# Kernel tuning notes

Hardware: AMD Instinct MI355X
Metric: run time of the kernel (lower is better)

## Reference

```python
import jax, jax.numpy as jnp
import numpy as np

H = 0.1  # spatial delta h from init kwargs


def _stencils():
    k_avg = jnp.array([[0., 0., 0.], [0., 1., 0.], [0., 0., 0.]], jnp.float32)
    k_x = (0.5 / H) * jnp.array([[0., -1., 0.], [0., 0., 0.], [0., 1., 0.]], jnp.float32)
    k_y = (0.5 / H) * jnp.array([[0., 0., 0.], [-1., 0., 1.], [0., 0., 0.]], jnp.float32)
    k_xx = (1.0 / H ** 2) * jnp.array([[0., 1., 0.], [0., -2., 0.], [0., 1., 0.]], jnp.float32)
    k_yy = (1.0 / H ** 2) * jnp.array([[0., 0., 0.], [1., -2., 1.], [0., 0., 0.]], jnp.float32)
    return k_avg, k_x, k_y, k_xx, k_yy


def setup_inputs() -> dict:
    key = jax.random.key(0)
    ks = jax.random.split(key, 11)
    B = 65536
    inp = {
        'data': jax.random.normal(ks[0], (B, 3, 11, 11), jnp.float32),
        'mix_a': jax.random.normal(ks[1], (128, 5 * 3 * 81), jnp.float32),
        'mix_b': jax.random.normal(ks[2], (128,), jnp.float32),
        'w1': jax.random.normal(ks[3], (128, 128), jnp.float32) * 0.08,
        'b1': jax.random.normal(ks[4], (128,), jnp.float32) * 0.05,
        'w2': jax.random.normal(ks[5], (128, 128), jnp.float32) * 0.08,
        'b2': jax.random.normal(ks[6], (128,), jnp.float32) * 0.05,
        'w3': jax.random.normal(ks[7], (128, 128), jnp.float32) * 0.08,
        'b3': jax.random.normal(ks[8], (128,), jnp.float32) * 0.05,
        'wf': jax.random.normal(ks[9], (5, 128), jnp.float32) * 0.08,
        'bf': jax.random.normal(ks[10], (5,), jnp.float32) * 0.05,
    }
    return inp


def reference(data, mix_a, mix_b, w1, b1, w2, b2, w3, b3, wf, bf):
    b = data.shape[0]
    # 3x3 patches over the 11x11 grid -> (b, c, 3, 3, 9, 9); last two dims are the
    # 9x9 valid output positions (l = n*9+m, matching torch unfold's reshape order).
    patches = jnp.stack(
        [jnp.stack([data[:, :, i:i + 9, j:j + 9] for j in range(3)], axis=2)
         for i in range(3)], axis=2)
    feats = [jnp.einsum('bcijnm,ij->bcnm', patches, k).reshape(b, -1)
             for k in _stencils()]  # each (b, 3*81)
    mixed = jnp.concatenate(feats, axis=1) @ mix_a.T + mix_b  # (b, 128)
    x = jnp.tanh(mixed)
    x = jnp.tanh(x @ w1.T + b1)
    x = jnp.tanh(x @ w2.T + b2)
    x = jnp.tanh(x @ w3.T + b3)
    return x @ wf.T + bf  # (b, 5)
```

## Files before the change

kernel.cpp:

```cpp
#include <hip/hip_runtime.h>
#include <hip/hip_bf16.h>

typedef __attribute__((ext_vector_type(4))) float f32x4;
typedef __attribute__((ext_vector_type(8))) short bf16x8;

#define MFMA(a,b,c) __builtin_amdgcn_mfma_f32_16x16x32_bf16((a),(b),(c),0,0,0)

__device__ inline void split_bf16(float a, unsigned short &h, unsigned short &l) {
    unsigned u = __float_as_uint(a);
    unsigned rh = (u + 0x7FFFu + ((u >> 16) & 1u)) & 0xFFFF0000u;
    float hf = __uint_as_float(rh);
    h = (unsigned short)(rh >> 16);
    float lf = a - hf;
    unsigned u2 = __float_as_uint(lf);
    l = (unsigned short)((u2 + 0x7FFFu + ((u2 >> 16) & 1u)) >> 16);
}

__device__ inline float tanh_fast(float x) {
    float e = __expf(2.f * x);
    return 1.f - 2.f * __builtin_amdgcn_rcpf(e + 1.f);
}

__device__ inline bf16x8 ldb(const unsigned short* p) { return *(const bf16x8*)p; }
__device__ inline f32x4 ld4u(const float* p) { f32x4 v; __builtin_memcpy(&v, p, 16); return v; }

__global__ void prep_all(const float* __restrict__ mix_a,
                         const float* __restrict__ w1, const float* __restrict__ w2,
                         const float* __restrict__ w3, const float* __restrict__ wf,
                         unsigned short* __restrict__ wph, unsigned short* __restrict__ wpl,
                         unsigned short* __restrict__ wlh, unsigned short* __restrict__ wll,
                         unsigned short* __restrict__ wfh, unsigned short* __restrict__ wfl) {
    int idx = blockIdx.x * 256 + threadIdx.x;
    if (idx < 128 * 384) {
        int o = idx / 384;
        int k = idx - o * 384;
        float acc = 0.f;
        if (k < 363) {
            int c = k / 121, rem = k - c * 121;
            int y = rem / 11, x = rem - y * 11;
            const float* ma = mix_a + (size_t)o * 1215 + c * 81;
            auto add = [&](int f, int i, int j, float coef) {
                int n = y - i, m = x - j;
                if (n >= 0 && n < 9 && m >= 0 && m < 9)
                    acc += ma[f * 243 + n * 9 + m] * coef;
            };
            add(0, 1, 1, 1.f);
            add(1, 0, 1, -5.f);  add(1, 2, 1, 5.f);
            add(2, 1, 0, -5.f);  add(2, 1, 2, 5.f);
            add(3, 0, 1, 100.f); add(3, 1, 1, -200.f); add(3, 2, 1, 100.f);
            add(4, 1, 0, 100.f); add(4, 1, 1, -200.f); add(4, 1, 2, 100.f);
        }
        unsigned short h, l; split_bf16(acc, h, l);
        int kt = k >> 5, ot = o >> 4;
        int lane = (o & 15) + 16 * ((k >> 3) & 3);
        int pidx = ((kt * 8 + ot) * 64 + lane) * 8 + (k & 7);
        wph[pidx] = h; wpl[pidx] = l;
        return;
    }
    idx -= 128 * 384;
    if (idx < 3 * 16384) {
        int layer = idx >> 14; int rem = idx & 16383;
        int o = rem >> 7, k = rem & 127;
        const float* w = (layer == 0) ? w1 : ((layer == 1) ? w2 : w3);
        float v = w[o * 128 + k];
        unsigned short h, l; split_bf16(v, h, l);
        int kt = k >> 5, ot = o >> 4;
        int lane = (o & 15) + 16 * ((k >> 3) & 3);
        int pidx = layer * 16384 + ((kt * 8 + ot) * 64 + lane) * 8 + (k & 7);
        wlh[pidx] = h; wll[pidx] = l;
    } else if (idx < 3 * 16384 + 2048) {
        int rem = idx - 3 * 16384;
        int o = rem >> 7, k = rem & 127;
        float v = (o < 5) ? wf[o * 128 + k] : 0.f;
        unsigned short h, l; split_bf16(v, h, l);
        int kt = k >> 5;
        int lane = (o & 15) + 16 * ((k >> 3) & 3);
        int pidx = (kt * 64 + lane) * 8 + (k & 7);
        wfh[pidx] = h; wfl[pidx] = l;
    }
}

__global__ __launch_bounds__(256, 2)
void fused_main(const float* __restrict__ data,
                const float* __restrict__ mix_b,
                const float* __restrict__ b1v,
                const float* __restrict__ b2v,
                const float* __restrict__ b3v,
                const float* __restrict__ bfv,
                const unsigned short* __restrict__ wp1h,
                const unsigned short* __restrict__ wp1l,
                const unsigned short* __restrict__ wlh,
                const unsigned short* __restrict__ wll,
                const unsigned short* __restrict__ wfh,
                const unsigned short* __restrict__ wfl,
                float* __restrict__ out, int Btot) {
    __shared__ __align__(16) unsigned short XsH[4][2][16][136];
    __shared__ __align__(16) unsigned short XsL[4][2][16][136];

    const int wave = threadIdx.x >> 6;
    const int lane = threadIdx.x & 63;
    const int s0 = (blockIdx.x * 4 + wave) * 32;
    if (s0 >= Btot) return;
    const int col = lane & 15;
    const int kg  = lane >> 4;

    const float* arow0 = data + (size_t)(s0 + col) * 363;
    const float* arow1 = arow0 + (size_t)16 * 363;

    f32x4 acc[2][8];
    #pragma unroll
    for (int ot = 0; ot < 8; ++ot) {
        float b = mix_b[col + 16 * ot];
        acc[0][ot] = (f32x4){b, b, b, b};
        acc[1][ot] = (f32x4){b, b, b, b};
    }

    bf16x8 bh[2][8], bl[8];
    f32x4 a4[2][2][2];
    a4[0][0][0] = ld4u(arow0 + kg * 8);     a4[0][0][1] = ld4u(arow0 + kg * 8 + 4);
    a4[0][1][0] = ld4u(arow1 + kg * 8);     a4[0][1][1] = ld4u(arow1 + kg * 8 + 4);
    #pragma unroll
    for (int ot = 0; ot < 8; ++ot)
        bh[0][ot] = ldb(wp1h + ((size_t)ot * 64 + lane) * 8);

    #pragma unroll
    for (int ktg = 0; ktg < 12; ++ktg) {
        const int p = ktg & 1;
        #pragma unroll
        for (int ot = 0; ot < 8; ++ot)
            bl[ot] = ldb(wp1l + (((size_t)(ktg * 8 + ot)) * 64 + lane) * 8);
        if (ktg < 11) {
            #pragma unroll
            for (int ot = 0; ot < 8; ++ot)
                bh[p ^ 1][ot] = ldb(wp1h + (((size_t)((ktg + 1) * 8 + ot)) * 64 + lane) * 8);
        }
        if (ktg < 10) {
            const int kb = (ktg + 1) * 32 + kg * 8;
            a4[p ^ 1][0][0] = ld4u(arow0 + kb); a4[p ^ 1][0][1] = ld4u(arow0 + kb + 4);
            a4[p ^ 1][1][0] = ld4u(arow1 + kb); a4[p ^ 1][1][1] = ld4u(arow1 + kb + 4);
        } else if (ktg == 10) {
            #pragma unroll
            for (int i = 0; i < 2; ++i)
                #pragma unroll
                for (int j = 0; j < 4; ++j) {
                    int k = 352 + kg * 8 + i * 4 + j;
                    bool ok = (k < 363);
                    a4[p ^ 1][0][i][j] = ok ? arow0[k] : 0.f;
                    a4[p ^ 1][1][i][j] = ok ? arow1[k] : 0.f;
                }
        }
        bf16x8 ah[2], al[2];
        #pragma unroll
        for (int t = 0; t < 2; ++t)
            #pragma unroll
            for (int i = 0; i < 2; ++i)
                #pragma unroll
                for (int j = 0; j < 4; ++j) {
                    unsigned short hh, ll;
                    split_bf16(a4[p][t][i][j], hh, ll);
                    ah[t][i * 4 + j] = (short)hh;
                    al[t][i * 4 + j] = (short)ll;
                }
        #pragma unroll
        for (int ot = 0; ot < 8; ++ot) {
            acc[0][ot] = MFMA(ah[0], bh[p][ot], acc[0][ot]);
            acc[1][ot] = MFMA(ah[1], bh[p][ot], acc[1][ot]);
        }
        #pragma unroll
        for (int ot = 0; ot < 8; ++ot) {
            acc[0][ot] = MFMA(al[0], bh[p][ot], acc[0][ot]);
            acc[1][ot] = MFMA(al[1], bh[p][ot], acc[1][ot]);
        }
        #pragma unroll
        for (int ot = 0; ot < 8; ++ot) {
            acc[0][ot] = MFMA(ah[0], bl[ot], acc[0][ot]);
            acc[1][ot] = MFMA(ah[1], bl[ot], acc[1][ot]);
        }
    }

    #pragma unroll
    for (int t = 0; t < 2; ++t)
        #pragma unroll
        for (int ot = 0; ot < 8; ++ot)
            #pragma unroll
            for (int j = 0; j < 4; ++j) {
                float x = tanh_fast(acc[t][ot][j]);
                unsigned short h, l; split_bf16(x, h, l);
                XsH[wave][t][kg * 4 + j][col + 16 * ot] = h;
                XsL[wave][t][kg * 4 + j][col + 16 * ot] = l;
            }

    const float* biases[3] = {b1v, b2v, b3v};
    bf16x8 lbh[2][8], lbl[8];
    asm volatile("s_waitcnt lgkmcnt(0)" ::: "memory");
    #pragma unroll
    for (int ot = 0; ot < 8; ++ot)
        lbh[0][ot] = ldb(wlh + ((size_t)ot * 64 + lane) * 8);

    #pragma unroll
    for (int layer = 0; layer < 3; ++layer) {
        const float* bb = biases[layer];
        f32x4 nacc[2][8];
        #pragma unroll
        for (int ot = 0; ot < 8; ++ot) {
            float b = bb[col + 16 * ot];
            nacc[0][ot] = (f32x4){b, b, b, b};
            nacc[1][ot] = (f32x4){b, b, b, b};
        }
        const unsigned short* pl0 = wll + (size_t)layer * 16384;
        #pragma unroll
        for (int kt = 0; kt < 4; ++kt) {
            const int s = layer * 4 + kt;
            const int p = s & 1;
            #pragma unroll
            for (int ot = 0; ot < 8; ++ot)
                lbl[ot] = ldb(pl0 + (((size_t)(kt * 8 + ot)) * 64 + lane) * 8);
            if (s < 11) {
                const int nl = (s + 1) >> 2, nk = (s + 1) & 3;
                const unsigned short* ph = wlh + (size_t)nl * 16384;
                #pragma unroll
                for (int ot = 0; ot < 8; ++ot)
                    lbh[p ^ 1][ot] = ldb(ph + (((size_t)(nk * 8 + ot)) * 64 + lane) * 8);
            }
            bf16x8 xh[2], xl[2];
            #pragma unroll
            for (int t = 0; t < 2; ++t) {
                xh[t] = *(const bf16x8*)&XsH[wave][t][col][kt * 32 + kg * 8];
                xl[t] = *(const bf16x8*)&XsL[wave][t][col][kt * 32 + kg * 8];
            }
            #pragma unroll
            for (int ot = 0; ot < 8; ++ot) {
                nacc[0][ot] = MFMA(xh[0], lbh[p][ot], nacc[0][ot]);
                nacc[1][ot] = MFMA(xh[1], lbh[p][ot], nacc[1][ot]);
            }
            #pragma unroll
            for (int ot = 0; ot < 8; ++ot) {
                nacc[0][ot] = MFMA(xl[0], lbh[p][ot], nacc[0][ot]);
                nacc[1][ot] = MFMA(xl[1], lbh[p][ot], nacc[1][ot]);
            }
            #pragma unroll
            for (int ot = 0; ot < 8; ++ot) {
                nacc[0][ot] = MFMA(xh[0], lbl[ot], nacc[0][ot]);
                nacc[1][ot] = MFMA(xh[1], lbl[ot], nacc[1][ot]);
            }
        }
        asm volatile("s_waitcnt lgkmcnt(0)" ::: "memory");
        #pragma unroll
        for (int t = 0; t < 2; ++t)
            #pragma unroll
            for (int ot = 0; ot < 8; ++ot)
                #pragma unroll
                for (int j = 0; j < 4; ++j) {
                    float x = tanh_fast(nacc[t][ot][j]);
                    unsigned short h, l; split_bf16(x, h, l);
                    XsH[wave][t][kg * 4 + j][col + 16 * ot] = h;
                    XsL[wave][t][kg * 4 + j][col + 16 * ot] = l;
                }
        asm volatile("s_waitcnt lgkmcnt(0)" ::: "memory");
    }

    float fb = (col < 5) ? bfv[col] : 0.f;
    f32x4 facc[2];
    facc[0] = (f32x4){fb, fb, fb, fb};
    facc[1] = (f32x4){fb, fb, fb, fb};
    #pragma unroll
    for (int kt = 0; kt < 4; ++kt) {
        bf16x8 fh = ldb(wfh + ((size_t)kt * 64 + lane) * 8);
        bf16x8 fl = ldb(wfl + ((size_t)kt * 64 + lane) * 8);
        #pragma unroll
        for (int t = 0; t < 2; ++t) {
            bf16x8 xh = *(const bf16x8*)&XsH[wave][t][col][kt * 32 + kg * 8];
            bf16x8 xl = *(const bf16x8*)&XsL[wave][t][col][kt * 32 + kg * 8];
            facc[t] = MFMA(xh, fh, facc[t]);
            facc[t] = MFMA(xl, fh, facc[t]);
            facc[t] = MFMA(xh, fl, facc[t]);
        }
    }
    if (col < 5) {
        #pragma unroll
        for (int t = 0; t < 2; ++t)
            #pragma unroll
            for (int j = 0; j < 4; ++j) {
                int s = s0 + 16 * t + kg * 4 + j;
                if (s < Btot) out[(size_t)s * 5 + col] = facc[t][j];
            }
    }
}

extern "C" void kernel_launch(void* const* d_in, const int* in_sizes, int n_in,
                              void* d_out, int out_size, void* d_ws, size_t ws_size,
                              hipStream_t stream) {
    const float* data  = (const float*)d_in[0];
    const float* mix_a = (const float*)d_in[1];
    const float* mix_b = (const float*)d_in[2];
    const float* w1    = (const float*)d_in[3];
    const float* b1    = (const float*)d_in[4];
    const float* w2    = (const float*)d_in[5];
    const float* b2    = (const float*)d_in[6];
    const float* w3    = (const float*)d_in[7];
    const float* b3    = (const float*)d_in[8];
    const float* wf    = (const float*)d_in[9];
    const float* bf    = (const float*)d_in[10];
    float* out = (float*)d_out;
    int Btot = in_sizes[0] / 363;

    if (ws_size < 401408) return;
    unsigned short* wp1h = (unsigned short*)d_ws;
    unsigned short* wp1l = wp1h + 49152;
    unsigned short* wlh  = wp1l + 49152;
    unsigned short* wll  = wlh + 49152;
    unsigned short* wfh  = wll + 49152;
    unsigned short* wfl  = wfh + 2048;

    prep_all<<<392, 256, 0, stream>>>(mix_a, w1, w2, w3, wf,
                                      wp1h, wp1l, wlh, wll, wfh, wfl);
    int blocks = (Btot + 127) / 128;
    fused_main<<<blocks, 256, 0, stream>>>(data, mix_b, b1, b2, b3, bf,
                                           wp1h, wp1l, wlh, wll, wfh, wfl, out, Btot);
}
```

Before: 207.0 us.

## Use single bf16 for hidden layers and halve rows per wave

```diff
diff --git a/kernel.cpp b/kernel.cpp
--- a/kernel.cpp
+++ b/kernel.cpp
@@ -16,6 +16,11 @@
     l = (unsigned short)((u2 + 0x7FFFu + ((u2 >> 16) & 1u)) >> 16);
 }
 
+__device__ inline unsigned short bf16_rn(float a) {
+    unsigned u = __float_as_uint(a);
+    return (unsigned short)((u + 0x7FFFu + ((u >> 16) & 1u)) >> 16);
+}
+
 __device__ inline float tanh_fast(float x) {
     float e = __expf(2.f * x);
     return 1.f - 2.f * __builtin_amdgcn_rcpf(e + 1.f);
@@ -28,8 +33,7 @@
                          const float* __restrict__ w1, const float* __restrict__ w2,
                          const float* __restrict__ w3, const float* __restrict__ wf,
                          unsigned short* __restrict__ wph, unsigned short* __restrict__ wpl,
-                         unsigned short* __restrict__ wlh, unsigned short* __restrict__ wll,
-                         unsigned short* __restrict__ wfh, unsigned short* __restrict__ wfl) {
+                         unsigned short* __restrict__ wlh, unsigned short* __restrict__ wfh) {
     int idx = blockIdx.x * 256 + threadIdx.x;
     if (idx < 128 * 384) {
         int o = idx / 384;
@@ -63,24 +67,22 @@
         int o = rem >> 7, k = rem & 127;
         const float* w = (layer == 0) ? w1 : ((layer == 1) ? w2 : w3);
         float v = w[o * 128 + k];
-        unsigned short h, l; split_bf16(v, h, l);
         int kt = k >> 5, ot = o >> 4;
         int lane = (o & 15) + 16 * ((k >> 3) & 3);
         int pidx = layer * 16384 + ((kt * 8 + ot) * 64 + lane) * 8 + (k & 7);
-        wlh[pidx] = h; wll[pidx] = l;
+        wlh[pidx] = bf16_rn(v);
     } else if (idx < 3 * 16384 + 2048) {
         int rem = idx - 3 * 16384;
         int o = rem >> 7, k = rem & 127;
         float v = (o < 5) ? wf[o * 128 + k] : 0.f;
-        unsigned short h, l; split_bf16(v, h, l);
         int kt = k >> 5;
         int lane = (o & 15) + 16 * ((k >> 3) & 3);
         int pidx = (kt * 64 + lane) * 8 + (k & 7);
-        wfh[pidx] = h; wfl[pidx] = l;
-    }
-}
-
-__global__ __launch_bounds__(256, 2)
+        wfh[pidx] = bf16_rn(v);
+    }
+}
+
+__global__ __launch_bounds__(256, 4)
 void fused_main(const float* __restrict__ data,
                 const float* __restrict__ mix_b,
                 const float* __restrict__ b1v,
@@ -90,54 +92,41 @@
                 const unsigned short* __restrict__ wp1h,
                 const unsigned short* __restrict__ wp1l,
                 const unsigned short* __restrict__ wlh,
-                const unsigned short* __restrict__ wll,
                 const unsigned short* __restrict__ wfh,
-                const unsigned short* __restrict__ wfl,
                 float* __restrict__ out, int Btot) {
-    __shared__ __align__(16) unsigned short XsH[4][2][16][136];
-    __shared__ __align__(16) unsigned short XsL[4][2][16][136];
+    __shared__ __align__(16) unsigned short XsH[4][16][136];
 
     const int wave = threadIdx.x >> 6;
     const int lane = threadIdx.x & 63;
-    const int s0 = (blockIdx.x * 4 + wave) * 32;
+    const int s0 = (blockIdx.x * 4 + wave) * 16;
     if (s0 >= Btot) return;
     const int col = lane & 15;
     const int kg  = lane >> 4;
 
-    const float* arow0 = data + (size_t)(s0 + col) * 363;
-    const float* arow1 = arow0 + (size_t)16 * 363;
-
-    f32x4 acc[2][8];
+    const float* arow = data + (size_t)(s0 + col) * 363;
+
+    f32x4 acc[8];
     #pragma unroll
     for (int ot = 0; ot < 8; ++ot) {
         float b = mix_b[col + 16 * ot];
-        acc[0][ot] = (f32x4){b, b, b, b};
-        acc[1][ot] = (f32x4){b, b, b, b};
-    }
-
-    bf16x8 bh[2][8], bl[8];
-    f32x4 a4[2][2][2];
-    a4[0][0][0] = ld4u(arow0 + kg * 8);     a4[0][0][1] = ld4u(arow0 + kg * 8 + 4);
-    a4[0][1][0] = ld4u(arow1 + kg * 8);     a4[0][1][1] = ld4u(arow1 + kg * 8 + 4);
-    #pragma unroll
-    for (int ot = 0; ot < 8; ++ot)
-        bh[0][ot] = ldb(wp1h + ((size_t)ot * 64 + lane) * 8);
+        acc[ot] = (f32x4){b, b, b, b};
+    }
+
+    bf16x8 bh[8];
+    f32x4 a4[2][2];
+    a4[0][0] = ld4u(arow + kg * 8);
+    a4[0][1] = ld4u(arow + kg * 8 + 4);
 
     #pragma unroll
     for (int ktg = 0; ktg < 12; ++ktg) {
         const int p = ktg & 1;
         #pragma unroll
         for (int ot = 0; ot < 8; ++ot)
-            bl[ot] = ldb(wp1l + (((size_t)(ktg * 8 + ot)) * 64 + lane) * 8);
-        if (ktg < 11) {
-            #pragma unroll
-            for (int ot = 0; ot < 8; ++ot)
-                bh[p ^ 1][ot] = ldb(wp1h + (((size_t)((ktg + 1) * 8 + ot)) * 64 + lane) * 8);
-        }
+            bh[ot] = ldb(wp1h + (((size_t)(ktg * 8 + ot)) * 64 + lane) * 8);
         if (ktg < 10) {
             const int kb = (ktg + 1) * 32 + kg * 8;
-            a4[p ^ 1][0][0] = ld4u(arow0 + kb); a4[p ^ 1][0][1] = ld4u(arow0 + kb + 4);
-            a4[p ^ 1][1][0] = ld4u(arow1 + kb); a4[p ^ 1][1][1] = ld4u(arow1 + kb + 4);
+            a4[p ^ 1][0] = ld4u(arow + kb);
+            a4[p ^ 1][1] = ld4u(arow + kb + 4);
         } else if (ktg == 10) {
             #pragma unroll
             for (int i = 0; i < 2; ++i)
@@ -145,76 +134,59 @@
                 for (int j = 0; j < 4; ++j) {
                     int k = 352 + kg * 8 + i * 4 + j;
                     bool ok = (k < 363);
-                    a4[p ^ 1][0][i][j] = ok ? arow0[k] : 0.f;
-                    a4[p ^ 1][1][i][j] = ok ? arow1[k] : 0.f;
+                    a4[p ^ 1][i][j] = ok ? arow[k] : 0.f;
                 }
         }
-        bf16x8 ah[2], al[2];
-        #pragma unroll
-        for (int t = 0; t < 2; ++t)
-            #pragma unroll
-            for (int i = 0; i < 2; ++i)
-                #pragma unroll
-                for (int j = 0; j < 4; ++j) {
-                    unsigned short hh, ll;
-                    split_bf16(a4[p][t][i][j], hh, ll);
-                    ah[t][i * 4 + j] = (short)hh;
-                    al[t][i * 4 + j] = (short)ll;
-                }
+        bf16x8 ah, al;
+        #pragma unroll
+        for (int i = 0; i < 2; ++i)
+            #pragma unroll
+            for (int j = 0; j < 4; ++j) {
+                unsigned short hh, ll;
+                split_bf16(a4[p][i][j], hh, ll);
+                ah[i * 4 + j] = (short)hh;
+                al[i * 4 + j] = (short)ll;
+            }
+        #pragma unroll
+        for (int ot = 0; ot < 8; ++ot)
+            acc[ot] = MFMA(ah, bh[ot], acc[ot]);
+        #pragma unroll
+        for (int ot = 0; ot < 8; ++ot)
+            acc[ot] = MFMA(al, bh[ot], acc[ot]);
         #pragma unroll
         for (int ot = 0; ot < 8; ++ot) {
-            acc[0][ot] = MFMA(ah[0], bh[p][ot], acc[0][ot]);
-            acc[1][ot] = MFMA(ah[1], bh[p][ot], acc[1][ot]);
-        }
-        #pragma unroll
-        for (int ot = 0; ot < 8; ++ot) {
-            acc[0][ot] = MFMA(al[0], bh[p][ot], acc[0][ot]);
-            acc[1][ot] = MFMA(al[1], bh[p][ot], acc[1][ot]);
-        }
-        #pragma unroll
-        for (int ot = 0; ot < 8; ++ot) {
-            acc[0][ot] = MFMA(ah[0], bl[ot], acc[0][ot]);
-            acc[1][ot] = MFMA(ah[1], bl[ot], acc[1][ot]);
-        }
-    }
-
-    #pragma unroll
-    for (int t = 0; t < 2; ++t)
-        #pragma unroll
-        for (int ot = 0; ot < 8; ++ot)
-            #pragma unroll
-            for (int j = 0; j < 4; ++j) {
-                float x = tanh_fast(acc[t][ot][j]);
-                unsigned short h, l; split_bf16(x, h, l);
-                XsH[wave][t][kg * 4 + j][col + 16 * ot] = h;
-                XsL[wave][t][kg * 4 + j][col + 16 * ot] = l;
-            }
-
-    const float* biases[3] = {b1v, b2v, b3v};
-    bf16x8 lbh[2][8], lbl[8];
-    asm volatile("s_waitcnt lgkmcnt(0)" ::: "memory");
+            bf16x8 bl = ldb(wp1l + (((size_t)(ktg * 8 + ot)) * 64 + lane) * 8);
+            acc[ot] = MFMA(ah, bl, acc[ot]);
+        }
+    }
+
+    bf16x8 lbh[2][8];
     #pragma unroll
     for (int ot = 0; ot < 8; ++ot)
         lbh[0][ot] = ldb(wlh + ((size_t)ot * 64 + lane) * 8);
 
     #pragma unroll
+    for (int ot = 0; ot < 8; ++ot)
+        #pragma unroll
+        for (int j = 0; j < 4; ++j)
+            XsH[wave][kg * 4 + j][col + 16 * ot] = bf16_rn(tanh_fast(acc[ot][j]));
+
+    const float* biases[3] = {b1v, b2v, b3v};
+    asm volatile("s_waitcnt lgkmcnt(0)" ::: "memory");
+
+    #pragma unroll
     for (int layer = 0; layer < 3; ++layer) {
         const float* bb = biases[layer];
-        f32x4 nacc[2][8];
+        f32x4 nacc[8];
         #pragma unroll
         for (int ot = 0; ot < 8; ++ot) {
             float b = bb[col + 16 * ot];
-            nacc[0][ot] = (f32x4){b, b, b, b};
-            nacc[1][ot] = (f32x4){b, b, b, b};
-        }
-        const unsigned short* pl0 = wll + (size_t)layer * 16384;
+            nacc[ot] = (f32x4){b, b, b, b};
+        }
         #pragma unroll
         for (int kt = 0; kt < 4; ++kt) {
             const int s = layer * 4 + kt;
             const int p = s & 1;
-            #pragma unroll
-            for (int ot = 0; ot < 8; ++ot)
-                lbl[ot] = ldb(pl0 + (((size_t)(kt * 8 + ot)) * 64 + lane) * 8);
             if (s < 11) {
                 const int nl = (s + 1) >> 2, nk = (s + 1) & 3;
                 const unsigned short* ph = wlh + (size_t)nl * 16384;
@@ -222,68 +194,34 @@
                 for (int ot = 0; ot < 8; ++ot)
                     lbh[p ^ 1][ot] = ldb(ph + (((size_t)(nk * 8 + ot)) * 64 + lane) * 8);
             }
-            bf16x8 xh[2], xl[2];
-            #pragma unroll
-            for (int t = 0; t < 2; ++t) {
-                xh[t] = *(const bf16x8*)&XsH[wave][t][col][kt * 32 + kg * 8];
-                xl[t] = *(const bf16x8*)&XsL[wave][t][col][kt * 32 + kg * 8];
-            }
-            #pragma unroll
-            for (int ot = 0; ot < 8; ++ot) {
-                nacc[0][ot] = MFMA(xh[0], lbh[p][ot], nacc[0][ot]);
-                nacc[1][ot] = MFMA(xh[1], lbh[p][ot], nacc[1][ot]);
-            }
-            #pragma unroll
-            for (int ot = 0; ot < 8; ++ot) {
-                nacc[0][ot] = MFMA(xl[0], lbh[p][ot], nacc[0][ot]);
-                nacc[1][ot] = MFMA(xl[1], lbh[p][ot], nacc[1][ot]);
-            }
-            #pragma unroll
-            for (int ot = 0; ot < 8; ++ot) {
-                nacc[0][ot] = MFMA(xh[0], lbl[ot], nacc[0][ot]);
-                nacc[1][ot] = MFMA(xh[1], lbl[ot], nacc[1][ot]);
-            }
+            bf16x8 xh = *(const bf16x8*)&XsH[wave][col][kt * 32 + kg * 8];
+            #pragma unroll
+            for (int ot = 0; ot < 8; ++ot)
+                nacc[ot] = MFMA(xh, lbh[p][ot], nacc[ot]);
         }
         asm volatile("s_waitcnt lgkmcnt(0)" ::: "memory");
         #pragma unroll
-        for (int t = 0; t < 2; ++t)
-            #pragma unroll
-            for (int ot = 0; ot < 8; ++ot)
-                #pragma unroll
-                for (int j = 0; j < 4; ++j) {
-                    float x = tanh_fast(nacc[t][ot][j]);
-                    unsigned short h, l; split_bf16(x, h, l);
-                    XsH[wave][t][kg * 4 + j][col + 16 * ot] = h;
-                    XsL[wave][t][kg * 4 + j][col + 16 * ot] = l;
-                }
+        for (int ot = 0; ot < 8; ++ot)
+            #pragma unroll
+            for (int j = 0; j < 4; ++j)
+                XsH[wave][kg * 4 + j][col + 16 * ot] = bf16_rn(tanh_fast(nacc[ot][j]));
         asm volatile("s_waitcnt lgkmcnt(0)" ::: "memory");
     }
 
     float fb = (col < 5) ? bfv[col] : 0.f;
-    f32x4 facc[2];
-    facc[0] = (f32x4){fb, fb, fb, fb};
-    facc[1] = (f32x4){fb, fb, fb, fb};
+    f32x4 facc = (f32x4){fb, fb, fb, fb};
     #pragma unroll
     for (int kt = 0; kt < 4; ++kt) {
         bf16x8 fh = ldb(wfh + ((size_t)kt * 64 + lane) * 8);
-        bf16x8 fl = ldb(wfl + ((size_t)kt * 64 + lane) * 8);
-        #pragma unroll
-        for (int t = 0; t < 2; ++t) {
-            bf16x8 xh = *(const bf16x8*)&XsH[wave][t][col][kt * 32 + kg * 8];
-            bf16x8 xl = *(const bf16x8*)&XsL[wave][t][col][kt * 32 + kg * 8];
-            facc[t] = MFMA(xh, fh, facc[t]);
-            facc[t] = MFMA(xl, fh, facc[t]);
-            facc[t] = MFMA(xh, fl, facc[t]);
-        }
+        bf16x8 xh = *(const bf16x8*)&XsH[wave][col][kt * 32 + kg * 8];
+        facc = MFMA(xh, fh, facc);
     }
     if (col < 5) {
         #pragma unroll
-        for (int t = 0; t < 2; ++t)
-            #pragma unroll
-            for (int j = 0; j < 4; ++j) {
-                int s = s0 + 16 * t + kg * 4 + j;
-                if (s < Btot) out[(size_t)s * 5 + col] = facc[t][j];
-            }
+        for (int j = 0; j < 4; ++j) {
+            int s = s0 + kg * 4 + j;
+            if (s < Btot) out[(size_t)s * 5 + col] = facc[j];
+        }
     }
 }
 
@@ -304,17 +242,15 @@
     float* out = (float*)d_out;
     int Btot = in_sizes[0] / 363;
 
-    if (ws_size < 401408) return;
+    if (ws_size < 299008) return;
     unsigned short* wp1h = (unsigned short*)d_ws;
     unsigned short* wp1l = wp1h + 49152;
     unsigned short* wlh  = wp1l + 49152;
-    unsigned short* wll  = wlh + 49152;
-    unsigned short* wfh  = wll + 49152;
-    unsigned short* wfl  = wfh + 2048;
+    unsigned short* wfh  = wlh + 49152;
 
     prep_all<<<392, 256, 0, stream>>>(mix_a, w1, w2, w3, wf,
-                                      wp1h, wp1l, wlh, wll, wfh, wfl);
-    int blocks = (Btot + 127) / 128;
+                                      wp1h, wp1l, wlh, wfh);
+    int blocks = (Btot + 63) / 64;
     fused_main<<<blocks, 256, 0, stream>>>(data, mix_b, b1, b2, b3, bf,
-                                           wp1h, wp1l, wlh, wll, wfh, wfl, out, Btot);
-}
+                                           wp1h, wp1l, wlh, wfh, out, Btot);
+}
```

Measured after the change: 204.9 us. About the same (-1.0%).
